# Kernel tuning notes

Hardware: AMD Instinct MI355X
Metric: run time of the kernel (lower is better)

The kernel has to match this reference:

```python
import jax, jax.numpy as jnp
import numpy as np

N = 50000        # nodes
E = 400000       # edges (no self-loops; self-loops appended in forward)
IN_DIM = 128
H, C = 4, 64     # heads, channels per head
D = H * C        # 256
NEG_SLOPE = 0.2


def setup_inputs() -> dict:
    key = jax.random.key(0)
    ks = jax.random.split(key, 8)
    x = jax.random.normal(ks[0], (N, IN_DIM), jnp.float32)
    # build edges with no self-loops (src != dst), matching the module's mask
    src = jax.random.randint(ks[1], (E,), 0, N)
    off = jax.random.randint(ks[2], (E,), 1, N)
    dst = (src + off) % N
    edge_index = jnp.stack([src, dst]).astype(jnp.int32)
    inp = {"x": x, "edge_index": edge_index}
    dims_in = [IN_DIM, D, D, D, D]
    for l in range(5):
        k = jax.random.split(ks[3 + l], 4)
        inp[f"W{l}"] = jax.random.normal(k[0], (D, dims_in[l]), jnp.float32) * 0.05
        inp[f"att_src{l}"] = jax.random.normal(k[1], (1, H, C), jnp.float32) * 0.05
        inp[f"att_dst{l}"] = jax.random.normal(k[2], (1, H, C), jnp.float32) * 0.05
        inp[f"bias{l}"] = jnp.zeros((D,), jnp.float32)
    return inp


def _gat_layer(x, W, a_src, a_dst, b, src, dst, relu_out):
    # linear projection, reshape to [N, H, C]
    h = (x @ W.T).reshape(N, H, C)
    alpha_src = jnp.sum(h * a_src, axis=-1)   # [N, H]
    alpha_dst = jnp.sum(h * a_dst, axis=-1)   # [N, H]
    # per-edge logits: alpha_j (source) + alpha_i (dest)
    alpha = jax.nn.leaky_relu(alpha_src[src] + alpha_dst[dst], negative_slope=NEG_SLOPE)  # [E', H]
    # segment softmax over destination neighborhoods (max is detached, as in the original)
    m = jax.lax.stop_gradient(jax.ops.segment_max(alpha, dst, num_segments=N))  # [N, H]
    e = jnp.exp(alpha - m[dst])
    s = jax.ops.segment_sum(e, dst, num_segments=N) + 1e-16
    a = e / s[dst]                                                             # [E', H]
    # weighted scatter-add aggregation of gathered source features
    out = jax.ops.segment_sum(a[:, :, None] * h[src], dst, num_segments=N)     # [N, H, C]
    out = out.reshape(N, D) + b
    return jax.nn.relu(out) if relu_out else out


def reference(x, edge_index,
              W0, att_src0, att_dst0, bias0,
              W1, att_src1, att_dst1, bias1,
              W2, att_src2, att_dst2, bias2,
              W3, att_src3, att_dst3, bias3,
              W4, att_src4, att_dst4, bias4):
    # input edges contain no self-loops; append one self-loop per node (as in the trace)
    loops = jnp.arange(N, dtype=edge_index.dtype)
    src = jnp.concatenate([edge_index[0], loops])
    dst = jnp.concatenate([edge_index[1], loops])
    params = [(W0, att_src0, att_dst0, bias0), (W1, att_src1, att_dst1, bias1),
              (W2, att_src2, att_dst2, bias2), (W3, att_src3, att_dst3, bias3),
              (W4, att_src4, att_dst4, bias4)]
    h = x
    for l, (W, a_s, a_d, b) in enumerate(params):
        h = _gat_layer(h, W, a_s, a_d, b, src, dst, relu_out=(l < 4))
    return h
```

## Files before the change

### kernel.cpp

```cpp
#include <hip/hip_runtime.h>
#include <hip/hip_bf16.h>

#define H 4
#define C 64
#define D 256
#define NEG_SLOPE 0.2f

typedef __attribute__((ext_vector_type(8))) _Float16 f16x8;
typedef __attribute__((ext_vector_type(4))) _Float16 f16x4;
typedef __attribute__((ext_vector_type(4))) float f32x4;

__global__ void k_cvt(const float* __restrict__ in, _Float16* __restrict__ out, int n4) {
    int i = blockIdx.x * blockDim.x + threadIdx.x;
    if (i >= n4) return;
    float4 v = ((const float4*)in)[i];
    f16x4 o = {(_Float16)v.x, (_Float16)v.y, (_Float16)v.z, (_Float16)v.w};
    *(f16x4*)&out[(size_t)i * 4] = o;
}

template<int K>
__global__ __launch_bounds__(256) void k_gemm_mfma(
        const _Float16* __restrict__ xf, const _Float16* __restrict__ wf,
        const float* __restrict__ att_src, const float* __restrict__ att_dst,
        _Float16* __restrict__ hmat, float* __restrict__ alpha_src,
        float* __restrict__ alpha_dst, int nrows) {
    __shared__ _Float16 sx[64][40];
    __shared__ _Float16 sw[256][40];
    int t = threadIdx.x;
    int w = t >> 6, l = t & 63;
    int r = l & 15, q = l >> 4;
    int row0 = blockIdx.x * 64;
    f32x4 acc[16];
    #pragma unroll
    for (int cf = 0; cf < 16; ++cf) acc[cf] = (f32x4){0.f, 0.f, 0.f, 0.f};

    int srow  = t >> 2;
    int sslot = t & 3;

    for (int k0 = 0; k0 < K; k0 += 32) {
        __syncthreads();
        {
            int gr = row0 + srow;
            uint4 v = make_uint4(0, 0, 0, 0);
            if (gr < nrows) v = *(const uint4*)&xf[(size_t)gr * K + k0 + sslot * 8];
            *(uint4*)&sx[srow][sslot * 8] = v;
        }
        #pragma unroll
        for (int i = 0; i < 4; ++i) {
            int wr = srow + i * 64;
            uint4 v = *(const uint4*)&wf[(size_t)wr * K + k0 + sslot * 8];
            *(uint4*)&sw[wr][sslot * 8] = v;
        }
        __syncthreads();
        f16x8 a = *(f16x8*)&sx[w * 16 + r][q * 8];
        #pragma unroll
        for (int cf = 0; cf < 16; ++cf) {
            f16x8 b = *(f16x8*)&sw[cf * 16 + r][q * 8];
            acc[cf] = __builtin_amdgcn_mfma_f32_16x16x32_f16(a, b, acc[cf], 0, 0, 0);
        }
    }
    #pragma unroll
    for (int cf = 0; cf < 16; ++cf) {
        #pragma unroll
        for (int i = 0; i < 4; ++i) {
            int gr = row0 + w * 16 + q * 4 + i;
            if (gr < nrows) hmat[(size_t)gr * D + cf * 16 + r] = (_Float16)acc[cf][i];
        }
    }
    float asv[16], adv[16];
    #pragma unroll
    for (int cf = 0; cf < 16; ++cf) {
        asv[cf] = att_src[cf * 16 + r];
        adv[cf] = att_dst[cf * 16 + r];
    }
    #pragma unroll
    for (int i = 0; i < 4; ++i) {
        #pragma unroll
        for (int h4 = 0; h4 < 4; ++h4) {
            float ps = 0.f, pd = 0.f;
            #pragma unroll
            for (int j = 0; j < 4; ++j) {
                int cf = h4 * 4 + j;
                ps += acc[cf][i] * asv[cf];
                pd += acc[cf][i] * adv[cf];
            }
            #pragma unroll
            for (int m = 1; m < 16; m <<= 1) {
                ps += __shfl_xor(ps, m);
                pd += __shfl_xor(pd, m);
            }
            int gr = row0 + w * 16 + q * 4 + i;
            if (r == 0 && gr < nrows) {
                alpha_src[gr * H + h4] = ps;
                alpha_dst[gr * H + h4] = pd;
            }
        }
    }
}

__global__ void k_deg(const int* __restrict__ ei, int E, int E2, int* __restrict__ deg) {
    int e = blockIdx.x * blockDim.x + threadIdx.x;
    if (e >= E2) return;
    int de = (e < E) ? ei[E + e] : (e - E);
    atomicAdd(&deg[de], 1);
}

__global__ void k_scan_block(const int* __restrict__ deg, int* __restrict__ incl,
                             int* __restrict__ bsum, int n) {
    __shared__ int sd[256];
    int t = threadIdx.x;
    int i = blockIdx.x * 256 + t;
    int v = (i < n) ? deg[i] : 0;
    sd[t] = v;
    __syncthreads();
    for (int off = 1; off < 256; off <<= 1) {
        int add = (t >= off) ? sd[t - off] : 0;
        __syncthreads();
        sd[t] += add;
        __syncthreads();
    }
    if (i < n) incl[i] = sd[t];
    if (t == 255) bsum[blockIdx.x] = sd[255];
}

__global__ void k_scan_bsum(int* __restrict__ bsum, int nb) {
    __shared__ int sd[256];
    int t = threadIdx.x;
    int v = (t < nb) ? bsum[t] : 0;
    sd[t] = v;
    __syncthreads();
    for (int off = 1; off < 256; off <<= 1) {
        int add = (t >= off) ? sd[t - off] : 0;
        __syncthreads();
        sd[t] += add;
        __syncthreads();
    }
    if (t < nb) bsum[t] = sd[t] - v;
}

__global__ void k_rowptr(const int* __restrict__ incl, const int* __restrict__ deg,
                         const int* __restrict__ boff, int* __restrict__ row_ptr,
                         int n, int total) {
    int i = blockIdx.x * blockDim.x + threadIdx.x;
    if (i < n) row_ptr[i] = incl[i] - deg[i] + boff[i >> 8];
    if (i == 0) row_ptr[n] = total;
}

__global__ void k_scatter(const int* __restrict__ ei, int E, int E2,
                          const int* __restrict__ row_ptr, int* __restrict__ cursor,
                          int* __restrict__ csr_src) {
    int e = blockIdx.x * blockDim.x + threadIdx.x;
    if (e >= E2) return;
    int se, de;
    if (e < E) { se = ei[e]; de = ei[E + e]; }
    else       { se = e - E; de = se; }
    int pos = atomicAdd(&cursor[de], 1);
    csr_src[row_ptr[de] + pos] = se;
}

__global__ __launch_bounds__(256) void k_aggregate(const _Float16* __restrict__ hmat,
        const int* __restrict__ row_ptr, const int* __restrict__ csr_src,
        const float* __restrict__ alpha_src, const float* __restrict__ alpha_dst,
        const float* __restrict__ bias, float* __restrict__ out_f32,
        _Float16* __restrict__ outx, int relu, int nrows) {
    int node = (blockIdx.x * 256 + threadIdx.x) >> 6;
    if (node >= nrows) return;
    int lane = threadIdx.x & 63;
    int hh   = lane >> 4;
    int c4   = lane * 4;
    int start = row_ptr[node], end = row_ptr[node + 1];
    float a_d = alpha_dst[node * H + hh];
    float4 acc = make_float4(0.f, 0.f, 0.f, 0.f);
    float ssum = 0.f;
    int i = start;
    for (; i + 8 <= end; i += 8) {
        int sn[8];
        #pragma unroll
        for (int j = 0; j < 8; ++j) sn[j] = csr_src[i + j];
        f16x4 hv[8];
        #pragma unroll
        for (int j = 0; j < 8; ++j)
            hv[j] = *(const f16x4*)&hmat[(size_t)sn[j] * D + c4];
        float as[8];
        #pragma unroll
        for (int j = 0; j < 8; ++j) as[j] = alpha_src[sn[j] * H + hh];
        #pragma unroll
        for (int j = 0; j < 8; ++j) {
            float a = as[j] + a_d;
            a = a > 0.f ? a : NEG_SLOPE * a;
            float ex = __expf(a);
            ssum += ex;
            acc.x += ex * (float)hv[j][0]; acc.y += ex * (float)hv[j][1];
            acc.z += ex * (float)hv[j][2]; acc.w += ex * (float)hv[j][3];
        }
    }
    for (; i < end; ++i) {
        int sn = csr_src[i];
        f16x4 hv = *(const f16x4*)&hmat[(size_t)sn * D + c4];
        float a = alpha_src[sn * H + hh] + a_d;
        a = a > 0.f ? a : NEG_SLOPE * a;
        float ex = __expf(a);
        ssum += ex;
        acc.x += ex * (float)hv[0]; acc.y += ex * (float)hv[1];
        acc.z += ex * (float)hv[2]; acc.w += ex * (float)hv[3];
    }
    float sinv = 1.f / (ssum + 1e-16f);
    float4 bv = *(const float4*)&bias[c4];
    float o[4];
    o[0] = acc.x * sinv + bv.x;
    o[1] = acc.y * sinv + bv.y;
    o[2] = acc.z * sinv + bv.z;
    o[3] = acc.w * sinv + bv.w;
    if (relu) {
        #pragma unroll
        for (int j = 0; j < 4; ++j) o[j] = fmaxf(o[j], 0.f);
    }
    if (outx) {
        f16x4 o4 = {(_Float16)o[0], (_Float16)o[1], (_Float16)o[2], (_Float16)o[3]};
        *(f16x4*)&outx[(size_t)node * D + c4] = o4;
    } else {
        *(float4*)&out_f32[(size_t)node * D + c4] =
            make_float4(o[0], o[1], o[2], o[3]);
    }
}

extern "C" void kernel_launch(void* const* d_in, const int* in_sizes, int n_in,
                              void* d_out, int out_size, void* d_ws, size_t ws_size,
                              hipStream_t stream) {
    const float* x = (const float*)d_in[0];
    const int* ei = (const int*)d_in[1];
    const int N  = in_sizes[0] / 128;
    const int E  = in_sizes[1] / 2;
    const int E2 = E + N;

    char* wsp = (char*)d_ws;
    size_t off = 0;
    auto alloc = [&](size_t bytes) -> void* {
        void* p = wsp + off;
        off += (bytes + 255) & ~(size_t)255;
        return p;
    };
    _Float16* bufH  = (_Float16*)alloc((size_t)N * D * 2);
    _Float16* xf16  = (_Float16*)alloc((size_t)N * D * 2);
    _Float16* wf16  = (_Float16*)alloc((size_t)5 * D * D * 2);
    float* alpha_src = (float*)alloc((size_t)N * H * 4);
    float* alpha_dst = (float*)alloc((size_t)N * H * 4);
    int*   deg       = (int*)alloc((size_t)N * 4);
    int*   incl      = (int*)alloc((size_t)N * 4);
    int*   bsum      = (int*)alloc(256 * 4);
    int*   row_ptr   = (int*)alloc((size_t)(N + 1) * 4);
    int*   cursor    = (int*)alloc((size_t)N * 4);
    int*   csr_src   = (int*)alloc((size_t)E2 * 4);
    (void)ws_size;

    hipMemsetAsync(deg, 0, (size_t)N * 4, stream);
    hipMemsetAsync(cursor, 0, (size_t)N * 4, stream);

    int nx4 = N * 128 / 4;
    k_cvt<<<(nx4 + 255) / 256, 256, 0, stream>>>(x, xf16, nx4);
    for (int l = 0; l < 5; ++l) {
        const float* W = (const float*)d_in[2 + 4 * l];
        int nw4 = D * (l == 0 ? 128 : 256) / 4;
        k_cvt<<<(nw4 + 255) / 256, 256, 0, stream>>>(W, wf16 + (size_t)l * D * D, nw4);
    }

    int egrid = (E2 + 255) / 256;
    k_deg<<<egrid, 256, 0, stream>>>(ei, E, E2, deg);
    int nb = (N + 255) / 256;
    k_scan_block<<<nb, 256, 0, stream>>>(deg, incl, bsum, N);
    k_scan_bsum<<<1, 256, 0, stream>>>(bsum, nb);
    k_rowptr<<<nb, 256, 0, stream>>>(incl, deg, bsum, row_ptr, N, E2);
    k_scatter<<<egrid, 256, 0, stream>>>(ei, E, E2, row_ptr, cursor, csr_src);

    int ggrid = (N + 63) / 64;
    int agrid = (N + 3) / 4;
    for (int l = 0; l < 5; ++l) {
        const float* as_ = (const float*)d_in[3 + 4 * l];
        const float* ad_ = (const float*)d_in[4 + 4 * l];
        const float* bs_ = (const float*)d_in[5 + 4 * l];
        const _Float16* wl = wf16 + (size_t)l * D * D;

        if (l == 0)
            k_gemm_mfma<128><<<ggrid, 256, 0, stream>>>(xf16, wl, as_, ad_,
                                                        bufH, alpha_src, alpha_dst, N);
        else
            k_gemm_mfma<256><<<ggrid, 256, 0, stream>>>(xf16, wl, as_, ad_,
                                                        bufH, alpha_src, alpha_dst, N);

        int last = (l == 4);
        k_aggregate<<<agrid, 256, 0, stream>>>(bufH, row_ptr, csr_src,
                                               alpha_src, alpha_dst, bs_,
                                               last ? (float*)d_out : nullptr,
                                               last ? nullptr : xf16,
                                               last ? 0 : 1, N);
    }
}
```

Measured before the change: 460.0 us.

## Split features into 32-channel planes and precompute edge softmax weights

Node features are stored as eight column planes of 32 halves each, and attention logits as per-head planes. A new per-node, per-head edge kernel computes the exp weights and row sums once. The aggregation grid then runs one block group per plane, so each gather touches a compact 64-byte row that fits in cache better. This adds an extra kernel, a 4×E2 weight buffer written and re-read every layer, and 8x more aggregate blocks, each reloading row_ptr and csr_src.

```diff
diff --git a/kernel.cpp b/kernel.cpp
--- a/kernel.cpp
+++ b/kernel.cpp
@@ -2,7 +2,6 @@
 #include <hip/hip_bf16.h>
 
 #define H 4
-#define C 64
 #define D 256
 #define NEG_SLOPE 0.2f
 
@@ -18,12 +17,27 @@
     *(f16x4*)&out[(size_t)i * 4] = o;
 }
 
+__global__ void k_cvt_x(const float* __restrict__ in, _Float16* __restrict__ xp,
+                        size_t pstride, int n) {
+    int i4 = blockIdx.x * blockDim.x + threadIdx.x;
+    if (i4 >= n * 32) return;
+    int row = i4 >> 5;
+    int q   = i4 & 31;
+    float4 v = ((const float4*)in)[i4];
+    f16x4 o = {(_Float16)v.x, (_Float16)v.y, (_Float16)v.z, (_Float16)v.w};
+    int plane = q >> 3;
+    int off   = (q & 7) * 4;
+    *(f16x4*)&xp[(size_t)plane * pstride + (size_t)row * 32 + off] = o;
+}
+
 template<int K>
 __global__ __launch_bounds__(256) void k_gemm_mfma(
-        const _Float16* __restrict__ xf, const _Float16* __restrict__ wf,
+        const _Float16* __restrict__ xp, size_t xpstride,
+        const _Float16* __restrict__ wf,
         const float* __restrict__ att_src, const float* __restrict__ att_dst,
-        _Float16* __restrict__ hmat, float* __restrict__ alpha_src,
-        float* __restrict__ alpha_dst, int nrows) {
+        _Float16* __restrict__ hp, size_t hpstride,
+        float* __restrict__ asp, float* __restrict__ adp, size_t apstride,
+        int nrows) {
     __shared__ _Float16 sx[64][40];
     __shared__ _Float16 sw[256][40];
     int t = threadIdx.x;
@@ -34,22 +48,18 @@
     #pragma unroll
     for (int cf = 0; cf < 16; ++cf) acc[cf] = (f32x4){0.f, 0.f, 0.f, 0.f};
 
-    int srow  = t >> 2;
-    int sslot = t & 3;
-
     for (int k0 = 0; k0 < K; k0 += 32) {
         __syncthreads();
         {
-            int gr = row0 + srow;
-            uint4 v = make_uint4(0, 0, 0, 0);
-            if (gr < nrows) v = *(const uint4*)&xf[(size_t)gr * K + k0 + sslot * 8];
-            *(uint4*)&sx[srow][sslot * 8] = v;
+            const _Float16* xsrc = xp + (size_t)(k0 >> 5) * xpstride + (size_t)row0 * 32;
+            uint4 v = *(const uint4*)(xsrc + (size_t)t * 8);
+            *(uint4*)&sx[t >> 2][(t & 3) * 8] = v;
         }
         #pragma unroll
         for (int i = 0; i < 4; ++i) {
-            int wr = srow + i * 64;
-            uint4 v = *(const uint4*)&wf[(size_t)wr * K + k0 + sslot * 8];
-            *(uint4*)&sw[wr][sslot * 8] = v;
+            int wr = (t >> 2) + i * 64;
+            uint4 v = *(const uint4*)&wf[(size_t)wr * K + k0 + (t & 3) * 8];
+            *(uint4*)&sw[wr][(t & 3) * 8] = v;
         }
         __syncthreads();
         f16x8 a = *(f16x8*)&sx[w * 16 + r][q * 8];
@@ -61,10 +71,12 @@
     }
     #pragma unroll
     for (int cf = 0; cf < 16; ++cf) {
+        _Float16* hpl = hp + (size_t)(cf >> 1) * hpstride;
         #pragma unroll
         for (int i = 0; i < 4; ++i) {
             int gr = row0 + w * 16 + q * 4 + i;
-            if (gr < nrows) hmat[(size_t)gr * D + cf * 16 + r] = (_Float16)acc[cf][i];
+            if (gr < nrows)
+                hpl[(size_t)gr * 32 + (cf & 1) * 16 + r] = (_Float16)acc[cf][i];
         }
     }
     float asv[16], adv[16];
@@ -91,8 +103,8 @@
             }
             int gr = row0 + w * 16 + q * 4 + i;
             if (r == 0 && gr < nrows) {
-                alpha_src[gr * H + h4] = ps;
-                alpha_dst[gr * H + h4] = pd;
+                asp[(size_t)h4 * apstride + gr] = ps;
+                adp[(size_t)h4 * apstride + gr] = pd;
             }
         }
     }
@@ -158,69 +170,79 @@
     csr_src[row_ptr[de] + pos] = se;
 }
 
-__global__ __launch_bounds__(256) void k_aggregate(const _Float16* __restrict__ hmat,
+__global__ void k_edge(const int* __restrict__ row_ptr, const int* __restrict__ csr_src,
+                       const float* __restrict__ asp, const float* __restrict__ adp,
+                       size_t apstride, float* __restrict__ ew, float* __restrict__ sp,
+                       int E2, int n) {
+    int node = blockIdx.x * blockDim.x + threadIdx.x;
+    if (node >= n) return;
+    int hd = blockIdx.y;
+    const float* aspp = asp + (size_t)hd * apstride;
+    float ad = adp[(size_t)hd * apstride + node];
+    float* ewp = ew + (size_t)hd * E2;
+    int st = row_ptr[node], en = row_ptr[node + 1];
+    float s = 0.f;
+    for (int i = st; i < en; ++i) {
+        float a = aspp[csr_src[i]] + ad;
+        a = a > 0.f ? a : NEG_SLOPE * a;
+        float w = __expf(a);
+        ewp[i] = w;
+        s += w;
+    }
+    sp[(size_t)hd * apstride + node] = s;
+}
+
+__global__ __launch_bounds__(256) void k_aggregate3(
+        const _Float16* __restrict__ hp, size_t hpstride,
         const int* __restrict__ row_ptr, const int* __restrict__ csr_src,
-        const float* __restrict__ alpha_src, const float* __restrict__ alpha_dst,
-        const float* __restrict__ bias, float* __restrict__ out_f32,
-        _Float16* __restrict__ outx, int relu, int nrows) {
-    int node = (blockIdx.x * 256 + threadIdx.x) >> 6;
+        const float* __restrict__ ew, const float* __restrict__ sp, size_t apstride,
+        const float* __restrict__ bias, float* __restrict__ outf,
+        _Float16* __restrict__ outx, size_t xpstride,
+        int E2, int relu, int nrows) {
+    int bid = blockIdx.x;
+    int cg = bid & 7;
+    int node = (bid >> 3) * 4 + (threadIdx.x >> 6);
     if (node >= nrows) return;
     int lane = threadIdx.x & 63;
-    int hh   = lane >> 4;
-    int c4   = lane * 4;
-    int start = row_ptr[node], end = row_ptr[node + 1];
-    float a_d = alpha_dst[node * H + hh];
-    float4 acc = make_float4(0.f, 0.f, 0.f, 0.f);
-    float ssum = 0.f;
-    int i = start;
-    for (; i + 8 <= end; i += 8) {
-        int sn[8];
-        #pragma unroll
-        for (int j = 0; j < 8; ++j) sn[j] = csr_src[i + j];
-        f16x4 hv[8];
-        #pragma unroll
-        for (int j = 0; j < 8; ++j)
-            hv[j] = *(const f16x4*)&hmat[(size_t)sn[j] * D + c4];
-        float as[8];
-        #pragma unroll
-        for (int j = 0; j < 8; ++j) as[j] = alpha_src[sn[j] * H + hh];
-        #pragma unroll
-        for (int j = 0; j < 8; ++j) {
-            float a = as[j] + a_d;
-            a = a > 0.f ? a : NEG_SLOPE * a;
-            float ex = __expf(a);
-            ssum += ex;
-            acc.x += ex * (float)hv[j][0]; acc.y += ex * (float)hv[j][1];
-            acc.z += ex * (float)hv[j][2]; acc.w += ex * (float)hv[j][3];
-        }
-    }
-    for (; i < end; ++i) {
-        int sn = csr_src[i];
-        f16x4 hv = *(const f16x4*)&hmat[(size_t)sn * D + c4];
-        float a = alpha_src[sn * H + hh] + a_d;
-        a = a > 0.f ? a : NEG_SLOPE * a;
-        float ex = __expf(a);
-        ssum += ex;
-        acc.x += ex * (float)hv[0]; acc.y += ex * (float)hv[1];
-        acc.z += ex * (float)hv[2]; acc.w += ex * (float)hv[3];
-    }
-    float sinv = 1.f / (ssum + 1e-16f);
-    float4 bv = *(const float4*)&bias[c4];
-    float o[4];
-    o[0] = acc.x * sinv + bv.x;
-    o[1] = acc.y * sinv + bv.y;
-    o[2] = acc.z * sinv + bv.z;
-    o[3] = acc.w * sinv + bv.w;
-    if (relu) {
-        #pragma unroll
-        for (int j = 0; j < 4; ++j) o[j] = fmaxf(o[j], 0.f);
-    }
-    if (outx) {
-        f16x4 o4 = {(_Float16)o[0], (_Float16)o[1], (_Float16)o[2], (_Float16)o[3]};
-        *(f16x4*)&outx[(size_t)node * D + c4] = o4;
-    } else {
-        *(float4*)&out_f32[(size_t)node * D + c4] =
-            make_float4(o[0], o[1], o[2], o[3]);
+    int half = lane >> 5;
+    int c    = lane & 31;
+    int head = cg >> 1;
+    const _Float16* hpl = hp + (size_t)cg * hpstride;
+    const float* ewp = ew + (size_t)head * E2;
+    int st = row_ptr[node], en = row_ptr[node + 1];
+    int deg = en - st;
+    float acc = 0.f;
+    for (int b = 0; b < deg; b += 64) {
+        int rem = deg - b; if (rem > 64) rem = 64;
+        int li = st + b + (lane < rem ? lane : rem - 1);
+        int myidx = csr_src[li];
+        float myw = (lane < rem) ? ewp[li] : 0.f;
+        for (int pb = 0; pb < rem; pb += 16) {
+            int sn[8]; float w[8];
+            #pragma unroll
+            for (int p = 0; p < 8; ++p) {
+                int e = pb + p * 2 + half;
+                int sl = e < rem ? e : rem - 1;
+                sn[p] = __shfl(myidx, sl);
+                float ww = __shfl(myw, sl);
+                w[p] = (e < rem) ? ww : 0.f;
+            }
+            _Float16 hv[8];
+            #pragma unroll
+            for (int p = 0; p < 8; ++p)
+                hv[p] = hpl[(size_t)sn[p] * 32 + c];
+            #pragma unroll
+            for (int p = 0; p < 8; ++p)
+                acc += w[p] * (float)hv[p];
+        }
+    }
+    acc += __shfl_xor(acc, 32);
+    float sinv = 1.f / (sp[(size_t)head * apstride + node] + 1e-16f);
+    float o = acc * sinv + bias[cg * 32 + c];
+    if (relu) o = fmaxf(o, 0.f);
+    if (half == 0) {
+        if (outx) outx[(size_t)cg * xpstride + (size_t)node * 32 + c] = (_Float16)o;
+        else      outf[(size_t)node * 256 + cg * 32 + c] = o;
     }
 }
 
@@ -232,6 +254,9 @@
     const int N  = in_sizes[0] / 128;
     const int E  = in_sizes[1] / 2;
     const int E2 = E + N;
+    const int Npad = (N + 63) & ~63;
+    const size_t PST = (size_t)Npad * 32;
+    const size_t AST = (size_t)Npad;
 
     char* wsp = (char*)d_ws;
     size_t off = 0;
@@ -240,24 +265,26 @@
         off += (bytes + 255) & ~(size_t)255;
         return p;
     };
-    _Float16* bufH  = (_Float16*)alloc((size_t)N * D * 2);
-    _Float16* xf16  = (_Float16*)alloc((size_t)N * D * 2);
-    _Float16* wf16  = (_Float16*)alloc((size_t)5 * D * D * 2);
-    float* alpha_src = (float*)alloc((size_t)N * H * 4);
-    float* alpha_dst = (float*)alloc((size_t)N * H * 4);
-    int*   deg       = (int*)alloc((size_t)N * 4);
-    int*   incl      = (int*)alloc((size_t)N * 4);
-    int*   bsum      = (int*)alloc(256 * 4);
-    int*   row_ptr   = (int*)alloc((size_t)(N + 1) * 4);
-    int*   cursor    = (int*)alloc((size_t)N * 4);
-    int*   csr_src   = (int*)alloc((size_t)E2 * 4);
+    _Float16* xp   = (_Float16*)alloc(8 * PST * 2);
+    _Float16* hp   = (_Float16*)alloc(8 * PST * 2);
+    _Float16* wf16 = (_Float16*)alloc((size_t)5 * D * D * 2);
+    float* asp = (float*)alloc(4 * AST * 4);
+    float* adp = (float*)alloc(4 * AST * 4);
+    float* sp  = (float*)alloc(4 * AST * 4);
+    float* ew  = (float*)alloc((size_t)4 * E2 * 4);
+    int* deg     = (int*)alloc((size_t)N * 4);
+    int* incl    = (int*)alloc((size_t)N * 4);
+    int* bsum    = (int*)alloc(256 * 4);
+    int* row_ptr = (int*)alloc((size_t)(N + 1) * 4);
+    int* cursor  = (int*)alloc((size_t)N * 4);
+    int* csr_src = (int*)alloc((size_t)E2 * 4);
     (void)ws_size;
 
     hipMemsetAsync(deg, 0, (size_t)N * 4, stream);
     hipMemsetAsync(cursor, 0, (size_t)N * 4, stream);
 
-    int nx4 = N * 128 / 4;
-    k_cvt<<<(nx4 + 255) / 256, 256, 0, stream>>>(x, xf16, nx4);
+    int nx4 = N * 32;
+    k_cvt_x<<<(nx4 + 255) / 256, 256, 0, stream>>>(x, xp, PST, N);
     for (int l = 0; l < 5; ++l) {
         const float* W = (const float*)d_in[2 + 4 * l];
         int nw4 = D * (l == 0 ? 128 : 256) / 4;
@@ -273,7 +300,8 @@
     k_scatter<<<egrid, 256, 0, stream>>>(ei, E, E2, row_ptr, cursor, csr_src);
 
     int ggrid = (N + 63) / 64;
-    int agrid = (N + 3) / 4;
+    int agrid = ((N + 3) / 4) * 8;
+    dim3 eg((N + 255) / 256, H);
     for (int l = 0; l < 5; ++l) {
         const float* as_ = (const float*)d_in[3 + 4 * l];
         const float* ad_ = (const float*)d_in[4 + 4 * l];
@@ -281,17 +309,18 @@
         const _Float16* wl = wf16 + (size_t)l * D * D;
 
         if (l == 0)
-            k_gemm_mfma<128><<<ggrid, 256, 0, stream>>>(xf16, wl, as_, ad_,
-                                                        bufH, alpha_src, alpha_dst, N);
+            k_gemm_mfma<128><<<ggrid, 256, 0, stream>>>(xp, PST, wl, as_, ad_,
+                                                        hp, PST, asp, adp, AST, N);
         else
-            k_gemm_mfma<256><<<ggrid, 256, 0, stream>>>(xf16, wl, as_, ad_,
-                                                        bufH, alpha_src, alpha_dst, N);
+            k_gemm_mfma<256><<<ggrid, 256, 0, stream>>>(xp, PST, wl, as_, ad_,
+                                                        hp, PST, asp, adp, AST, N);
+
+        k_edge<<<eg, 256, 0, stream>>>(row_ptr, csr_src, asp, adp, AST, ew, sp, E2, N);
 
         int last = (l == 4);
-        k_aggregate<<<agrid, 256, 0, stream>>>(bufH, row_ptr, csr_src,
-                                               alpha_src, alpha_dst, bs_,
-                                               last ? (float*)d_out : nullptr,
-                                               last ? nullptr : xf16,
-                                               last ? 0 : 1, N);
-    }
-}
+        k_aggregate3<<<agrid, 256, 0, stream>>>(hp, PST, row_ptr, csr_src, ew, sp, AST,
+                                                bs_, last ? (float*)d_out : nullptr,
+                                                last ? nullptr : xp, PST,
+                                                E2, last ? 0 : 1, N);
+    }
+}
```

After: 850.0 us. 1.85x slower.

## Split neighbor edges across half-waves with 16-byte feature gathers; fuse conversions

Applied to the files above, without the earlier changes.

The aggregation kernel now splits each wavefront into two 32-lane halves. Each half processes 8 edges per iteration and each lane gathers 8 fp16 channels (16 bytes), and the two partial sums are combined with a cross-half shuffle. Out-of-range edges in a block are clamped and masked, which removes the scalar tail loop. The six fp32-to-fp16 conversion launches are merged into one kernel with a packed weight layout, which cuts launch overhead. In exchange, low-degree nodes spend wasted lanes on masked edges.

```diff
diff --git a/kernel.cpp b/kernel.cpp
--- a/kernel.cpp
+++ b/kernel.cpp
@@ -2,7 +2,6 @@
 #include <hip/hip_bf16.h>
 
 #define H 4
-#define C 64
 #define D 256
 #define NEG_SLOPE 0.2f
 
@@ -10,12 +9,34 @@
 typedef __attribute__((ext_vector_type(4))) _Float16 f16x4;
 typedef __attribute__((ext_vector_type(4))) float f32x4;
 
-__global__ void k_cvt(const float* __restrict__ in, _Float16* __restrict__ out, int n4) {
+__global__ void k_cvt_all(const float* __restrict__ x,
+                          const float* __restrict__ w0, const float* __restrict__ w1,
+                          const float* __restrict__ w2, const float* __restrict__ w3,
+                          const float* __restrict__ w4,
+                          _Float16* __restrict__ xf, _Float16* __restrict__ wf,
+                          int nx4) {
     int i = blockIdx.x * blockDim.x + threadIdx.x;
-    if (i >= n4) return;
-    float4 v = ((const float4*)in)[i];
+    const int nW0 = 128 * 256 / 4, nW = 256 * 256 / 4;
+    const float* src;
+    _Float16* dst;
+    int off;
+    if (i < nx4) { src = x; dst = xf; off = i; }
+    else {
+        i -= nx4;
+        if (i < nW0) { src = w0; dst = wf; off = i; }
+        else {
+            i -= nW0;
+            int l = i / nW, r2 = i % nW;
+            if (l >= 4) return;
+            const float* ws[4] = {w1, w2, w3, w4};
+            src = ws[l];
+            dst = wf + 128 * 256 + (size_t)l * 256 * 256;
+            off = r2;
+        }
+    }
+    float4 v = ((const float4*)src)[off];
     f16x4 o = {(_Float16)v.x, (_Float16)v.y, (_Float16)v.z, (_Float16)v.w};
-    *(f16x4*)&out[(size_t)i * 4] = o;
+    *(f16x4*)&dst[(size_t)off * 4] = o;
 }
 
 template<int K>
@@ -34,22 +55,19 @@
     #pragma unroll
     for (int cf = 0; cf < 16; ++cf) acc[cf] = (f32x4){0.f, 0.f, 0.f, 0.f};
 
-    int srow  = t >> 2;
-    int sslot = t & 3;
-
     for (int k0 = 0; k0 < K; k0 += 32) {
         __syncthreads();
         {
-            int gr = row0 + srow;
+            int gr = row0 + (t >> 2);
             uint4 v = make_uint4(0, 0, 0, 0);
-            if (gr < nrows) v = *(const uint4*)&xf[(size_t)gr * K + k0 + sslot * 8];
-            *(uint4*)&sx[srow][sslot * 8] = v;
+            if (gr < nrows) v = *(const uint4*)&xf[(size_t)gr * K + k0 + (t & 3) * 8];
+            *(uint4*)&sx[t >> 2][(t & 3) * 8] = v;
         }
         #pragma unroll
         for (int i = 0; i < 4; ++i) {
-            int wr = srow + i * 64;
-            uint4 v = *(const uint4*)&wf[(size_t)wr * K + k0 + sslot * 8];
-            *(uint4*)&sw[wr][sslot * 8] = v;
+            int wr = (t >> 2) + i * 64;
+            uint4 v = *(const uint4*)&wf[(size_t)wr * K + k0 + (t & 3) * 8];
+            *(uint4*)&sw[wr][(t & 3) * 8] = v;
         }
         __syncthreads();
         f16x8 a = *(f16x8*)&sx[w * 16 + r][q * 8];
@@ -91,8 +109,8 @@
             }
             int gr = row0 + w * 16 + q * 4 + i;
             if (r == 0 && gr < nrows) {
-                alpha_src[gr * H + h4] = ps;
-                alpha_dst[gr * H + h4] = pd;
+                alpha_src[gr * 4 + h4] = ps;
+                alpha_dst[gr * 4 + h4] = pd;
             }
         }
     }
@@ -161,66 +179,71 @@
 __global__ __launch_bounds__(256) void k_aggregate(const _Float16* __restrict__ hmat,
         const int* __restrict__ row_ptr, const int* __restrict__ csr_src,
         const float* __restrict__ alpha_src, const float* __restrict__ alpha_dst,
-        const float* __restrict__ bias, float* __restrict__ out_f32,
+        const float* __restrict__ bias, float* __restrict__ outf,
         _Float16* __restrict__ outx, int relu, int nrows) {
     int node = (blockIdx.x * 256 + threadIdx.x) >> 6;
     if (node >= nrows) return;
     int lane = threadIdx.x & 63;
-    int hh   = lane >> 4;
-    int c4   = lane * 4;
-    int start = row_ptr[node], end = row_ptr[node + 1];
-    float a_d = alpha_dst[node * H + hh];
-    float4 acc = make_float4(0.f, 0.f, 0.f, 0.f);
+    int e2 = lane >> 5;
+    int c  = lane & 31;
+    int head = c >> 3;
+    int st = row_ptr[node], en = row_ptr[node + 1];
+    int deg = en - st;
+    float a_d = alpha_dst[node * 4 + head];
+    float acc[8] = {};
     float ssum = 0.f;
-    int i = start;
-    for (; i + 8 <= end; i += 8) {
+    for (int b = 0; b < deg; b += 16) {
         int sn[8];
         #pragma unroll
-        for (int j = 0; j < 8; ++j) sn[j] = csr_src[i + j];
-        f16x4 hv[8];
+        for (int j = 0; j < 8; ++j) {
+            int e = b + e2 * 8 + j;
+            int li = st + (e < deg ? e : deg - 1);
+            sn[j] = csr_src[li];
+        }
+        f16x8 hv[8];
         #pragma unroll
         for (int j = 0; j < 8; ++j)
-            hv[j] = *(const f16x4*)&hmat[(size_t)sn[j] * D + c4];
+            hv[j] = *(const f16x8*)&hmat[(size_t)sn[j] * D + c * 8];
         float as[8];
         #pragma unroll
-        for (int j = 0; j < 8; ++j) as[j] = alpha_src[sn[j] * H + hh];
+        for (int j = 0; j < 8; ++j) as[j] = alpha_src[sn[j] * 4 + head];
         #pragma unroll
         for (int j = 0; j < 8; ++j) {
+            int e = b + e2 * 8 + j;
             float a = as[j] + a_d;
             a = a > 0.f ? a : NEG_SLOPE * a;
-            float ex = __expf(a);
+            float ex = (e < deg) ? __expf(a) : 0.f;
             ssum += ex;
-            acc.x += ex * (float)hv[j][0]; acc.y += ex * (float)hv[j][1];
-            acc.z += ex * (float)hv[j][2]; acc.w += ex * (float)hv[j][3];
-        }
-    }
-    for (; i < end; ++i) {
-        int sn = csr_src[i];
-        f16x4 hv = *(const f16x4*)&hmat[(size_t)sn * D + c4];
-        float a = alpha_src[sn * H + hh] + a_d;
-        a = a > 0.f ? a : NEG_SLOPE * a;
-        float ex = __expf(a);
-        ssum += ex;
-        acc.x += ex * (float)hv[0]; acc.y += ex * (float)hv[1];
-        acc.z += ex * (float)hv[2]; acc.w += ex * (float)hv[3];
-    }
-    float sinv = 1.f / (ssum + 1e-16f);
-    float4 bv = *(const float4*)&bias[c4];
-    float o[4];
-    o[0] = acc.x * sinv + bv.x;
-    o[1] = acc.y * sinv + bv.y;
-    o[2] = acc.z * sinv + bv.z;
-    o[3] = acc.w * sinv + bv.w;
-    if (relu) {
-        #pragma unroll
-        for (int j = 0; j < 4; ++j) o[j] = fmaxf(o[j], 0.f);
-    }
-    if (outx) {
-        f16x4 o4 = {(_Float16)o[0], (_Float16)o[1], (_Float16)o[2], (_Float16)o[3]};
-        *(f16x4*)&outx[(size_t)node * D + c4] = o4;
-    } else {
-        *(float4*)&out_f32[(size_t)node * D + c4] =
-            make_float4(o[0], o[1], o[2], o[3]);
+            #pragma unroll
+            for (int k = 0; k < 8; ++k) acc[k] += ex * (float)hv[j][k];
+        }
+    }
+    ssum += __shfl_xor(ssum, 32);
+    #pragma unroll
+    for (int k = 0; k < 8; ++k) acc[k] += __shfl_xor(acc[k], 32);
+    if (e2 == 0) {
+        float sinv = 1.f / (ssum + 1e-16f);
+        float4 b0 = *(const float4*)&bias[c * 8];
+        float4 b1 = *(const float4*)&bias[c * 8 + 4];
+        float o[8];
+        o[0] = acc[0] * sinv + b0.x; o[1] = acc[1] * sinv + b0.y;
+        o[2] = acc[2] * sinv + b0.z; o[3] = acc[3] * sinv + b0.w;
+        o[4] = acc[4] * sinv + b1.x; o[5] = acc[5] * sinv + b1.y;
+        o[6] = acc[6] * sinv + b1.z; o[7] = acc[7] * sinv + b1.w;
+        if (relu) {
+            #pragma unroll
+            for (int k = 0; k < 8; ++k) o[k] = fmaxf(o[k], 0.f);
+        }
+        if (outx) {
+            f16x8 o8 = {(_Float16)o[0], (_Float16)o[1], (_Float16)o[2], (_Float16)o[3],
+                        (_Float16)o[4], (_Float16)o[5], (_Float16)o[6], (_Float16)o[7]};
+            *(f16x8*)&outx[(size_t)node * D + c * 8] = o8;
+        } else {
+            *(float4*)&outf[(size_t)node * D + c * 8] =
+                make_float4(o[0], o[1], o[2], o[3]);
+            *(float4*)&outf[(size_t)node * D + c * 8 + 4] =
+                make_float4(o[4], o[5], o[6], o[7]);
+        }
     }
 }
 
@@ -242,7 +265,7 @@
     };
     _Float16* bufH  = (_Float16*)alloc((size_t)N * D * 2);
     _Float16* xf16  = (_Float16*)alloc((size_t)N * D * 2);
-    _Float16* wf16  = (_Float16*)alloc((size_t)5 * D * D * 2);
+    _Float16* wf16  = (_Float16*)alloc((size_t)(128 * 256 + 4 * 256 * 256) * 2);
     float* alpha_src = (float*)alloc((size_t)N * H * 4);
     float* alpha_dst = (float*)alloc((size_t)N * H * 4);
     int*   deg       = (int*)alloc((size_t)N * 4);
@@ -257,12 +280,10 @@
     hipMemsetAsync(cursor, 0, (size_t)N * 4, stream);
 
     int nx4 = N * 128 / 4;
-    k_cvt<<<(nx4 + 255) / 256, 256, 0, stream>>>(x, xf16, nx4);
-    for (int l = 0; l < 5; ++l) {
-        const float* W = (const float*)d_in[2 + 4 * l];
-        int nw4 = D * (l == 0 ? 128 : 256) / 4;
-        k_cvt<<<(nw4 + 255) / 256, 256, 0, stream>>>(W, wf16 + (size_t)l * D * D, nw4);
-    }
+    int tot4 = nx4 + 128 * 256 / 4 + 4 * (256 * 256 / 4);
+    k_cvt_all<<<(tot4 + 255) / 256, 256, 0, stream>>>(
+        x, (const float*)d_in[2], (const float*)d_in[6], (const float*)d_in[10],
+        (const float*)d_in[14], (const float*)d_in[18], xf16, wf16, nx4);
 
     int egrid = (E2 + 255) / 256;
     k_deg<<<egrid, 256, 0, stream>>>(ei, E, E2, deg);
@@ -278,7 +299,8 @@
         const float* as_ = (const float*)d_in[3 + 4 * l];
         const float* ad_ = (const float*)d_in[4 + 4 * l];
         const float* bs_ = (const float*)d_in[5 + 4 * l];
-        const _Float16* wl = wf16 + (size_t)l * D * D;
+        const _Float16* wl = (l == 0) ? wf16
+                           : wf16 + 128 * 256 + (size_t)(l - 1) * 256 * 256;
 
         if (l == 0)
             k_gemm_mfma<128><<<ggrid, 256, 0, stream>>>(xf16, wl, as_, ad_,
```

New measurement: 430.0 us. 6.5% less time.
